# Kernel tuning notes

Hardware: AMD Instinct MI355X
Metric: run time of the kernel (lower is better)

## Reference

```python
import jax, jax.numpy as jnp
import numpy as np


def _extract_patches(img, p, s):
    # img: [B,H,W,C] -> [B,PY,PX,p,p,C]
    B, H, W, C = img.shape
    PY = (H - p) // s + 1
    PX = (W - p) // s + 1
    ar = jnp.arange(p)
    rows = jnp.arange(PY) * s
    cols = jnp.arange(PX) * s
    a = img[:, rows[:, None] + ar]              # [B,PY,p,W,C]
    b = a[:, :, :, cols[:, None] + ar]          # [B,PY,p,PX,p,C]
    return b.transpose(0, 1, 3, 2, 4, 5)


def _extract_shifted(img, int_prior, p, s):
    # img: [B,H,W,C], int_prior: [B,PY,PX,2] (dy,dx) -> shifted patches + validity
    B, H, W, C = img.shape
    _, PY, PX, _ = int_prior.shape
    ar = jnp.arange(p)
    sy = jnp.arange(PY)[None, :, None] * s + int_prior[..., 0]   # [B,PY,PX]
    sx = jnp.arange(PX)[None, None, :] * s + int_prior[..., 1]
    valid = (sy >= 0) & (sy <= H - p) & (sx >= 0) & (sx <= W - p)
    sy = jnp.clip(sy, 0, H - p)
    sx = jnp.clip(sx, 0, W - p)
    ridx = sy[..., None] + ar                                    # [B,PY,PX,p]
    cidx = sx[..., None] + ar
    bidx = jnp.arange(B)[:, None, None, None, None]
    patches = img[bidx, ridx[..., :, None], cidx[..., None, :]]  # [B,PY,PX,p,p,C]
    return patches, valid


def _patch_flow_loss(p1, p2, flow, p):
    # bilinear-warp p2 by per-patch subpixel flow and compare to p1 -> [B,PY,PX]
    ar = jnp.arange(p, dtype=flow.dtype)
    y = ar + flow[..., 0:1]                                      # [B,PY,PX,p]
    x = ar + flow[..., 1:2]
    y0 = jnp.clip(jnp.floor(y), 0, p - 1).astype(jnp.int32)
    x0 = jnp.clip(jnp.floor(x), 0, p - 1).astype(jnp.int32)
    y1 = jnp.clip(y0 + 1, 0, p - 1)
    x1 = jnp.clip(x0 + 1, 0, p - 1)
    wy = jnp.clip(y - y0, 0.0, 1.0)[..., :, None, None]
    wx = jnp.clip(x - x0, 0.0, 1.0)[..., None, :, None]
    r0 = jnp.take_along_axis(p2, y0[..., :, None, None], axis=3)
    r1 = jnp.take_along_axis(p2, y1[..., :, None, None], axis=3)
    v00 = jnp.take_along_axis(r0, x0[..., None, :, None], axis=4)
    v01 = jnp.take_along_axis(r0, x1[..., None, :, None], axis=4)
    v10 = jnp.take_along_axis(r1, x0[..., None, :, None], axis=4)
    v11 = jnp.take_along_axis(r1, x1[..., None, :, None], axis=4)
    warped = (1 - wy) * ((1 - wx) * v00 + wx * v01) + wy * ((1 - wx) * v10 + wx * v11)
    return jnp.mean((warped - p1) ** 2, axis=(3, 4, 5))


def setup_inputs() -> dict:
    key = jax.random.key(0)
    ks = jax.random.split(key, 5)
    B, H, W, C = 16, 512, 512, 3
    p, s = 16, 8
    PY = (H - p) // s + 1
    PX = (W - p) // s + 1
    hidden = 512
    din = 2 * p * p * C + 2
    img1 = jax.random.normal(ks[0], (B, H, W, C), dtype=jnp.float32)
    img2 = jax.random.normal(ks[1], (B, H, W, C), dtype=jnp.float32)
    prior = jax.random.normal(ks[2], (B, PY, PX, 2), dtype=jnp.float32) * 2.0
    w1 = jax.random.normal(ks[3], (din, hidden), dtype=jnp.float32) / np.sqrt(din)
    b1 = jnp.zeros((hidden,), jnp.float32)
    w2 = jax.random.normal(ks[4], (hidden, 2), dtype=jnp.float32) / np.sqrt(hidden)
    b2 = jnp.zeros((2,), jnp.float32)
    return {"img1": img1, "img2": img2, "prior": prior, "w1": w1, "b1": b1,
            "w2": w2, "b2": b2, "patch_size": p, "stride": s}


def reference(img1, img2, prior, w1, b1, w2, b2, patch_size, stride):
    p, s = patch_size, stride
    B, PY, PX, _ = prior.shape
    patches1 = _extract_patches(img1, p, s)                       # [B,PY,PX,p,p,C]
    int_priors = jnp.round(jax.lax.stop_gradient(prior)).astype(jnp.int32)
    remainder = prior - int_priors
    patches2, _valid = _extract_shifted(img2, int_priors, p, s)   # validity unused downstream
    N = B * PY * PX
    feat = jnp.concatenate([patches1.reshape(N, -1),
                            patches2.reshape(N, -1),
                            remainder.reshape(N, 2)], axis=-1)
    h = jax.nn.relu(feat @ w1 + b1)
    residual = (h @ w2 + b2).reshape(B, PY, PX, 2)
    remainder_flow = remainder + residual
    flow = int_priors + remainder_flow
    loss = _patch_flow_loss(patches1, patches2, remainder_flow, p)[..., None]
    return jnp.concatenate([flow, loss], axis=-1)                 # [B,PY,PX,3]
```

## Files before the change

kernel.cpp:

```cpp
#include <hip/hip_runtime.h>

#define BQ   16
#define HH   512
#define WW   512
#define CC   3
#define PSZ  16
#define STR  8
#define PYN  63
#define PXN  63
#define NPATCH (BQ * PYN * PXN)
#define HID  512
#define MT   48
#define NTH  1024
#define KSTEPS 48

typedef __attribute__((ext_vector_type(8))) short  short8;
typedef __attribute__((ext_vector_type(4))) float  f32x4;

__device__ __forceinline__ ushort f2bf(float f) {
    unsigned u = __float_as_uint(f);
    u = (u + 0x7fffu + ((u >> 16) & 1u)) >> 16;
    return (ushort)u;
}
__device__ __forceinline__ float bf2f(ushort h) {
    return __uint_as_float(((unsigned)h) << 16);
}
__device__ __forceinline__ unsigned pk2(float a, float b) {
    return (unsigned)f2bf(a) | ((unsigned)f2bf(b) << 16);
}

__global__ void pack_w1_kernel(const float* __restrict__ w1, ushort* __restrict__ w1p) {
    int e = blockIdx.x * 256 + threadIdx.x;
    int k = e >> 9;
    int n = e & 511;
    int idx = ((k >> 5) << 14) + ((n >> 4) << 9) + (((k >> 3) & 3) << 7) + ((n & 15) << 3) + (k & 7);
    w1p[idx] = f2bf(w1[e]);
}

__global__ __launch_bounds__(NTH)
void lfe_mfma_kernel(const float* __restrict__ img1,
                     const float* __restrict__ img2,
                     const float* __restrict__ prior,
                     const float* __restrict__ w1,
                     const float* __restrict__ b1,
                     const float* __restrict__ w2,
                     const float* __restrict__ b2,
                     const ushort* __restrict__ w1p,
                     float* __restrict__ out)
{
    __shared__ ushort feat[3 * KSTEPS * 512];
    __shared__ float  red[16][MT][2];
    __shared__ float  srem[MT][2];
    __shared__ float  sflow[MT][2];
    __shared__ int    sip[MT][2];
    __shared__ int    sbase1[MT];
    __shared__ int    sbase2[MT];

    const int t    = threadIdx.x;
    const int wid  = t >> 6;
    const int lane = t & 63;
    const int n0   = blockIdx.x * MT;

    const int ntb = wid << 1;
    const ushort* bbase = w1p + ((size_t)lane << 3);
    short8 B0[2], B1[2];
    #define LOADB(B, s_) {                                            \
        const ushort* p_ = bbase + ((size_t)(((s_) << 5) + ntb) << 9);\
        B[0] = *(const short8*)(p_);                                  \
        B[1] = *(const short8*)(p_ + 512);                            \
    }
    LOADB(B0, 0);
    LOADB(B1, 1);

    if (t < MT) {
        int n = n0 + t;
        float py_ = prior[(size_t)n * 2 + 0];
        float px_ = prior[(size_t)n * 2 + 1];
        int ipy = (int)rintf(py_);
        int ipx = (int)rintf(px_);
        sip[t][0] = ipy; sip[t][1] = ipx;
        srem[t][0] = py_ - (float)ipy;
        srem[t][1] = px_ - (float)ipx;
        int b  = n / (PYN * PXN);
        int r  = n % (PYN * PXN);
        int py = r / PXN, px = r % PXN;
        int by = py * STR, bx = px * STR;
        int sy = min(max(by + ipy, 0), HH - PSZ);
        int sx = min(max(bx + ipx, 0), WW - PSZ);
        sbase1[t] = ((b * HH + by) * WW + bx) * CC;
        sbase2[t] = ((b * HH + sy) * WW + sx) * CC;
    }
    __syncthreads();

    {
        const int plo = lane >> 2;
        const int kk2 = lane & 3;
        #pragma unroll 4
        for (int i = 0; i < 36; ++i) {
            int c = (i << 4) + wid;
            int m = c / 192;
            int r = c - m * 192;
            int s = r >> 2, g = r & 3;
            int pi = (m << 4) + plo;
            int ka = (s << 5) + (g << 3) + (kk2 << 1);
            const float* src;
            int e;
            if (ka < 768) { src = img1 + sbase1[pi]; e = ka; }
            else          { src = img2 + sbase2[pi]; e = ka - 768; }
            int yi  = e / 48;
            int off = e - yi * 48;
            const float* g8 = src + yi * (WW * CC) + off;
            float va = g8[0], vb = g8[1];
            int idx = ((m * KSTEPS + s) << 9) + (g << 7) + (plo << 3) + (kk2 << 1);
            *(unsigned*)(&feat[idx]) = pk2(va, vb);
        }
    }
    __syncthreads();

    const int cn = lane & 15;
    const int g  = lane >> 4;

    f32x4 acc[3][2];
    #pragma unroll
    for (int m = 0; m < 3; ++m)
        #pragma unroll
        for (int nt = 0; nt < 2; ++nt) acc[m][nt] = f32x4{0.f, 0.f, 0.f, 0.f};

    const ushort* fb = feat + lane * 8;

    for (int s = 0; s < KSTEPS; s += 2) {
        {
            short8 A0 = *(const short8*)(fb + ((0 * KSTEPS + s) << 9));
            short8 A1 = *(const short8*)(fb + ((1 * KSTEPS + s) << 9));
            short8 A2 = *(const short8*)(fb + ((2 * KSTEPS + s) << 9));
            #pragma unroll
            for (int nt = 0; nt < 2; ++nt) {
                acc[0][nt] = __builtin_amdgcn_mfma_f32_16x16x32_bf16(A0, B0[nt], acc[0][nt], 0, 0, 0);
                acc[1][nt] = __builtin_amdgcn_mfma_f32_16x16x32_bf16(A1, B0[nt], acc[1][nt], 0, 0, 0);
                acc[2][nt] = __builtin_amdgcn_mfma_f32_16x16x32_bf16(A2, B0[nt], acc[2][nt], 0, 0, 0);
            }
        }
        int sa = (s + 2 < KSTEPS) ? s + 2 : KSTEPS - 1;
        LOADB(B0, sa);
        {
            short8 A0 = *(const short8*)(fb + ((0 * KSTEPS + s + 1) << 9));
            short8 A1 = *(const short8*)(fb + ((1 * KSTEPS + s + 1) << 9));
            short8 A2 = *(const short8*)(fb + ((2 * KSTEPS + s + 1) << 9));
            #pragma unroll
            for (int nt = 0; nt < 2; ++nt) {
                acc[0][nt] = __builtin_amdgcn_mfma_f32_16x16x32_bf16(A0, B1[nt], acc[0][nt], 0, 0, 0);
                acc[1][nt] = __builtin_amdgcn_mfma_f32_16x16x32_bf16(A1, B1[nt], acc[1][nt], 0, 0, 0);
                acc[2][nt] = __builtin_amdgcn_mfma_f32_16x16x32_bf16(A2, B1[nt], acc[2][nt], 0, 0, 0);
            }
        }
        int sb = (s + 3 < KSTEPS) ? s + 3 : KSTEPS - 1;
        LOADB(B1, sb);
    }
    #undef LOADB

    float ps[3][4][2];
    #pragma unroll
    for (int m = 0; m < 3; ++m)
        #pragma unroll
        for (int r = 0; r < 4; ++r) { ps[m][r][0] = 0.f; ps[m][r][1] = 0.f; }

    #pragma unroll
    for (int nt = 0; nt < 2; ++nt) {
        int j = (wid << 5) + (nt << 4) + cn;
        float w1a = w1[(size_t)1536 * HID + j];
        float w1b = w1[(size_t)1537 * HID + j];
        float bb  = b1[j];
        float w20 = w2[(size_t)j * 2 + 0];
        float w21 = w2[(size_t)j * 2 + 1];
        #pragma unroll
        for (int m = 0; m < 3; ++m) {
            #pragma unroll
            for (int r = 0; r < 4; ++r) {
                int pr = (m << 4) + (g << 2) + r;
                float h = acc[m][nt][r] + bb + srem[pr][0] * w1a + srem[pr][1] * w1b;
                h = fmaxf(h, 0.f);
                ps[m][r][0] = fmaf(h, w20, ps[m][r][0]);
                ps[m][r][1] = fmaf(h, w21, ps[m][r][1]);
            }
        }
    }
    #pragma unroll
    for (int m = 0; m < 3; ++m)
        #pragma unroll
        for (int r = 0; r < 4; ++r)
            #pragma unroll
            for (int cc = 0; cc < 2; ++cc)
                #pragma unroll
                for (int off = 1; off < 16; off <<= 1)
                    ps[m][r][cc] += __shfl_xor(ps[m][r][cc], off, 64);
    if (cn == 0) {
        #pragma unroll
        for (int m = 0; m < 3; ++m)
            #pragma unroll
            for (int r = 0; r < 4; ++r) {
                int pr = (m << 4) + (g << 2) + r;
                red[wid][pr][0] = ps[m][r][0];
                red[wid][pr][1] = ps[m][r][1];
            }
    }
    __syncthreads();
    if (t < MT * 2) {
        int pr = t >> 1, c = t & 1;
        float v = b2[c];
        #pragma unroll
        for (int w = 0; w < 16; ++w) v += red[w][pr][c];
        sflow[pr][c] = srem[pr][c] + v;
    }
    __syncthreads();

    {
        const int gi = t >> 4, lt = t & 15;
        if (gi < MT) {
            const int pi = gi;
            const float rfy = sflow[pi][0], rfx = sflow[pi][1];
            const int pbase = (pi >> 4) * 24576 + ((pi & 15) << 3);
            float lsum = 0.f;

            const int xj = lt;
            float x  = (float)xj + rfx;
            int   x0 = min(max((int)floorf(x), 0), PSZ - 1);
            int   x1 = min(x0 + 1, PSZ - 1);
            float wx = fminf(fmaxf(x - (float)x0, 0.f), 1.f);
            int   c0 = x0 * 3, c1 = x1 * 3;
            #pragma unroll 4
            for (int yi = 0; yi < PSZ; ++yi) {
                float y  = (float)yi + rfy;
                int   y0 = min(max((int)floorf(y), 0), PSZ - 1);
                int   y1 = min(y0 + 1, PSZ - 1);
                float wy = fminf(fmaxf(y - (float)y0, 0.f), 1.f);
                int r0 = 768 + y0 * 48, r1 = 768 + y1 * 48;
                int ep = yi * 48 + xj * 3;
                #pragma unroll
                for (int cc = 0; cc < 3; ++cc) {
                    int k00 = r0 + c0 + cc, k01 = r0 + c1 + cc;
                    int k10 = r1 + c0 + cc, k11 = r1 + c1 + cc;
                    float v00 = bf2f(feat[pbase + ((k00 >> 3) << 7) + (k00 & 7)]);
                    float v01 = bf2f(feat[pbase + ((k01 >> 3) << 7) + (k01 & 7)]);
                    float v10 = bf2f(feat[pbase + ((k10 >> 3) << 7) + (k10 & 7)]);
                    float v11 = bf2f(feat[pbase + ((k11 >> 3) << 7) + (k11 & 7)]);
                    float a = v00 + wx * (v01 - v00);
                    float b = v10 + wx * (v11 - v10);
                    float warped = a + wy * (b - a);
                    int kp = ep + cc;
                    float d = warped - bf2f(feat[pbase + ((kp >> 3) << 7) + (kp & 7)]);
                    lsum = fmaf(d, d, lsum);
                }
            }
            #pragma unroll
            for (int off = 1; off < 16; off <<= 1)
                lsum += __shfl_xor(lsum, off, 64);

            if (lt == 0) {
                int n = n0 + pi;
                out[(size_t)n * 3 + 0] = (float)sip[pi][0] + rfy;
                out[(size_t)n * 3 + 1] = (float)sip[pi][1] + rfx;
                out[(size_t)n * 3 + 2] = lsum * (1.f / 768.f);
            }
        }
    }
}

extern "C" void kernel_launch(void* const* d_in, const int* in_sizes, int n_in,
                              void* d_out, int out_size, void* d_ws, size_t ws_size,
                              hipStream_t stream) {
    const float* img1  = (const float*)d_in[0];
    const float* img2  = (const float*)d_in[1];
    const float* prior = (const float*)d_in[2];
    const float* w1    = (const float*)d_in[3];
    const float* b1    = (const float*)d_in[4];
    const float* w2    = (const float*)d_in[5];
    const float* b2    = (const float*)d_in[6];
    float* out = (float*)d_out;
    ushort* w1p = (ushort*)d_ws;

    pack_w1_kernel<<<dim3((1536 * HID) / 256), dim3(256), 0, stream>>>(w1, w1p);

    dim3 grid(NPATCH / MT);
    dim3 block(NTH);
    lfe_mfma_kernel<<<grid, block, 0, stream>>>(img1, img2, prior, w1, b1, w2, b2, w1p, out);
}
```

Before: 403.5 us.

## Halve patches per block with XOR-swizzled LDS layout and split loss rows

The patch tile per block drops from 48 to 24. The LDS feature buffer shrinks and is laid out as one 16-row tile plus a half-height 8-row tile, so fewer MFMA and A-loads run per k-step and more blocks can fit per CU. An XOR swizzle is added to the LDS feature indices to cut bank conflicts on A-fragment reads and on the warp-loss gathers. The loss stage now spreads each patch over 32 threads, splitting the rows in halves. In exchange, each w1 B fragment is reused across fewer patches, so global/L2 traffic for weights doubles per patch, and the second MFMA tile wastes half its rows.

```diff
diff --git a/kernel.cpp b/kernel.cpp
--- a/kernel.cpp
+++ b/kernel.cpp
@@ -10,9 +10,10 @@
 #define PXN  63
 #define NPATCH (BQ * PYN * PXN)
 #define HID  512
-#define MT   48
+#define MT   24
 #define NTH  1024
 #define KSTEPS 48
+#define M1BASE 24576
 
 typedef __attribute__((ext_vector_type(8))) short  short8;
 typedef __attribute__((ext_vector_type(4))) float  f32x4;
@@ -27,6 +28,12 @@
 }
 __device__ __forceinline__ unsigned pk2(float a, float b) {
     return (unsigned)f2bf(a) | ((unsigned)f2bf(b) << 16);
+}
+
+__device__ __forceinline__ int fidx(int pi, int k) {
+    int B = k >> 3, kk = k & 7;
+    if (pi < 16) return (B << 7) + ((pi ^ (B & 15)) << 3) + kk;
+    return M1BASE + (B << 6) + (((pi - 16) ^ (B & 7)) << 3) + kk;
 }
 
 __global__ void pack_w1_kernel(const float* __restrict__ w1, ushort* __restrict__ w1p) {
@@ -37,7 +44,7 @@
     w1p[idx] = f2bf(w1[e]);
 }
 
-__global__ __launch_bounds__(NTH)
+__global__ __launch_bounds__(NTH, 8)
 void lfe_mfma_kernel(const float* __restrict__ img1,
                      const float* __restrict__ img2,
                      const float* __restrict__ prior,
@@ -48,7 +55,7 @@
                      const ushort* __restrict__ w1p,
                      float* __restrict__ out)
 {
-    __shared__ ushort feat[3 * KSTEPS * 512];
+    __shared__ ushort feat[36864];
     __shared__ float  red[16][MT][2];
     __shared__ float  srem[MT][2];
     __shared__ float  sflow[MT][2];
@@ -64,10 +71,10 @@
     const int ntb = wid << 1;
     const ushort* bbase = w1p + ((size_t)lane << 3);
     short8 B0[2], B1[2];
-    #define LOADB(B, s_) {                                            \
+    #define LOADB(Bv, s_) {                                           \
         const ushort* p_ = bbase + ((size_t)(((s_) << 5) + ntb) << 9);\
-        B[0] = *(const short8*)(p_);                                  \
-        B[1] = *(const short8*)(p_ + 512);                            \
+        Bv[0] = *(const short8*)(p_);                                 \
+        Bv[1] = *(const short8*)(p_ + 512);                           \
     }
     LOADB(B0, 0);
     LOADB(B1, 1);
@@ -96,23 +103,33 @@
         const int plo = lane >> 2;
         const int kk2 = lane & 3;
         #pragma unroll 4
-        for (int i = 0; i < 36; ++i) {
-            int c = (i << 4) + wid;
-            int m = c / 192;
-            int r = c - m * 192;
-            int s = r >> 2, g = r & 3;
-            int pi = (m << 4) + plo;
-            int ka = (s << 5) + (g << 3) + (kk2 << 1);
-            const float* src;
-            int e;
-            if (ka < 768) { src = img1 + sbase1[pi]; e = ka; }
-            else          { src = img2 + sbase2[pi]; e = ka - 768; }
-            int yi  = e / 48;
-            int off = e - yi * 48;
-            const float* g8 = src + yi * (WW * CC) + off;
-            float va = g8[0], vb = g8[1];
-            int idx = ((m * KSTEPS + s) << 9) + (g << 7) + (plo << 3) + (kk2 << 1);
-            *(unsigned*)(&feat[idx]) = pk2(va, vb);
+        for (int i = 0; i < 24; ++i) {
+            int c  = (i << 4) + wid;
+            int m1 = (c >= 192);
+            int r  = c - (m1 ? 192 : 0);
+            int s  = r >> 2, g = r & 3;
+            int Bb = (s << 2) + g;
+            bool active = true;
+            int pi, idx;
+            if (!m1) {
+                pi  = plo;
+                idx = (s << 9) + (g << 7) + (((plo) ^ (Bb & 15)) << 3) + (kk2 << 1);
+            } else {
+                active = (plo < 8);
+                pi  = 16 + (plo & 7);
+                idx = M1BASE + (s << 8) + (g << 6) + ((((plo) & 7) ^ (Bb & 7)) << 3) + (kk2 << 1);
+            }
+            if (active) {
+                int ka = (s << 5) + (g << 3) + (kk2 << 1);
+                const float* src;
+                int e;
+                if (ka < 768) { src = img1 + sbase1[pi]; e = ka; }
+                else          { src = img2 + sbase2[pi]; e = ka - 768; }
+                int yi  = e / 48;
+                int off = e - yi * 48;
+                const float* g8 = src + yi * (WW * CC) + off;
+                *(unsigned*)(&feat[idx]) = pk2(g8[0], g8[1]);
+            }
         }
     }
     __syncthreads();
@@ -120,37 +137,34 @@
     const int cn = lane & 15;
     const int g  = lane >> 4;
 
-    f32x4 acc[3][2];
+    f32x4 acc[2][2];
     #pragma unroll
-    for (int m = 0; m < 3; ++m)
+    for (int m = 0; m < 2; ++m)
         #pragma unroll
         for (int nt = 0; nt < 2; ++nt) acc[m][nt] = f32x4{0.f, 0.f, 0.f, 0.f};
-
-    const ushort* fb = feat + lane * 8;
 
     for (int s = 0; s < KSTEPS; s += 2) {
         {
-            short8 A0 = *(const short8*)(fb + ((0 * KSTEPS + s) << 9));
-            short8 A1 = *(const short8*)(fb + ((1 * KSTEPS + s) << 9));
-            short8 A2 = *(const short8*)(fb + ((2 * KSTEPS + s) << 9));
+            int Bb = (s << 2) + g;
+            short8 A0 = *(const short8*)(feat + (s << 9) + (g << 7) + ((cn ^ (Bb & 15)) << 3));
+            short8 A1 = *(const short8*)(feat + M1BASE + (s << 8) + (g << 6) + (((lane & 7) ^ (Bb & 7)) << 3));
             #pragma unroll
             for (int nt = 0; nt < 2; ++nt) {
                 acc[0][nt] = __builtin_amdgcn_mfma_f32_16x16x32_bf16(A0, B0[nt], acc[0][nt], 0, 0, 0);
                 acc[1][nt] = __builtin_amdgcn_mfma_f32_16x16x32_bf16(A1, B0[nt], acc[1][nt], 0, 0, 0);
-                acc[2][nt] = __builtin_amdgcn_mfma_f32_16x16x32_bf16(A2, B0[nt], acc[2][nt], 0, 0, 0);
             }
         }
         int sa = (s + 2 < KSTEPS) ? s + 2 : KSTEPS - 1;
         LOADB(B0, sa);
         {
-            short8 A0 = *(const short8*)(fb + ((0 * KSTEPS + s + 1) << 9));
-            short8 A1 = *(const short8*)(fb + ((1 * KSTEPS + s + 1) << 9));
-            short8 A2 = *(const short8*)(fb + ((2 * KSTEPS + s + 1) << 9));
+            int s1 = s + 1;
+            int Bb = (s1 << 2) + g;
+            short8 A0 = *(const short8*)(feat + (s1 << 9) + (g << 7) + ((cn ^ (Bb & 15)) << 3));
+            short8 A1 = *(const short8*)(feat + M1BASE + (s1 << 8) + (g << 6) + (((lane & 7) ^ (Bb & 7)) << 3));
             #pragma unroll
             for (int nt = 0; nt < 2; ++nt) {
                 acc[0][nt] = __builtin_amdgcn_mfma_f32_16x16x32_bf16(A0, B1[nt], acc[0][nt], 0, 0, 0);
                 acc[1][nt] = __builtin_amdgcn_mfma_f32_16x16x32_bf16(A1, B1[nt], acc[1][nt], 0, 0, 0);
-                acc[2][nt] = __builtin_amdgcn_mfma_f32_16x16x32_bf16(A2, B1[nt], acc[2][nt], 0, 0, 0);
             }
         }
         int sb = (s + 3 < KSTEPS) ? s + 3 : KSTEPS - 1;
@@ -158,9 +172,9 @@
     }
     #undef LOADB
 
-    float ps[3][4][2];
+    float ps[2][4][2];
     #pragma unroll
-    for (int m = 0; m < 3; ++m)
+    for (int m = 0; m < 2; ++m)
         #pragma unroll
         for (int r = 0; r < 4; ++r) { ps[m][r][0] = 0.f; ps[m][r][1] = 0.f; }
 
@@ -173,19 +187,21 @@
         float w20 = w2[(size_t)j * 2 + 0];
         float w21 = w2[(size_t)j * 2 + 1];
         #pragma unroll
-        for (int m = 0; m < 3; ++m) {
+        for (int m = 0; m < 2; ++m) {
             #pragma unroll
             for (int r = 0; r < 4; ++r) {
                 int pr = (m << 4) + (g << 2) + r;
-                float h = acc[m][nt][r] + bb + srem[pr][0] * w1a + srem[pr][1] * w1b;
-                h = fmaxf(h, 0.f);
-                ps[m][r][0] = fmaf(h, w20, ps[m][r][0]);
-                ps[m][r][1] = fmaf(h, w21, ps[m][r][1]);
+                if (pr < MT) {
+                    float h = acc[m][nt][r] + bb + srem[pr][0] * w1a + srem[pr][1] * w1b;
+                    h = fmaxf(h, 0.f);
+                    ps[m][r][0] = fmaf(h, w20, ps[m][r][0]);
+                    ps[m][r][1] = fmaf(h, w21, ps[m][r][1]);
+                }
             }
         }
     }
     #pragma unroll
-    for (int m = 0; m < 3; ++m)
+    for (int m = 0; m < 2; ++m)
         #pragma unroll
         for (int r = 0; r < 4; ++r)
             #pragma unroll
@@ -195,12 +211,14 @@
                     ps[m][r][cc] += __shfl_xor(ps[m][r][cc], off, 64);
     if (cn == 0) {
         #pragma unroll
-        for (int m = 0; m < 3; ++m)
+        for (int m = 0; m < 2; ++m)
             #pragma unroll
             for (int r = 0; r < 4; ++r) {
                 int pr = (m << 4) + (g << 2) + r;
-                red[wid][pr][0] = ps[m][r][0];
-                red[wid][pr][1] = ps[m][r][1];
+                if (pr < MT) {
+                    red[wid][pr][0] = ps[m][r][0];
+                    red[wid][pr][1] = ps[m][r][1];
+                }
             }
     }
     __syncthreads();
@@ -214,21 +232,24 @@
     __syncthreads();
 
     {
-        const int gi = t >> 4, lt = t & 15;
+        const int gi = t >> 5;
+        const int lt = t & 31;
         if (gi < MT) {
             const int pi = gi;
             const float rfy = sflow[pi][0], rfx = sflow[pi][1];
-            const int pbase = (pi >> 4) * 24576 + ((pi & 15) << 3);
-            float lsum = 0.f;
-
-            const int xj = lt;
+            const int xj = lt & 15;
+            const int yh = lt >> 4;
+
             float x  = (float)xj + rfx;
             int   x0 = min(max((int)floorf(x), 0), PSZ - 1);
             int   x1 = min(x0 + 1, PSZ - 1);
             float wx = fminf(fmaxf(x - (float)x0, 0.f), 1.f);
             int   c0 = x0 * 3, c1 = x1 * 3;
-            #pragma unroll 4
-            for (int yi = 0; yi < PSZ; ++yi) {
+
+            float lsum = 0.f;
+            #pragma unroll
+            for (int yy = 0; yy < 8; ++yy) {
+                int yi = (yh << 3) + yy;
                 float y  = (float)yi + rfy;
                 int   y0 = min(max((int)floorf(y), 0), PSZ - 1);
                 int   y1 = min(y0 + 1, PSZ - 1);
@@ -237,22 +258,19 @@
                 int ep = yi * 48 + xj * 3;
                 #pragma unroll
                 for (int cc = 0; cc < 3; ++cc) {
-                    int k00 = r0 + c0 + cc, k01 = r0 + c1 + cc;
-                    int k10 = r1 + c0 + cc, k11 = r1 + c1 + cc;
-                    float v00 = bf2f(feat[pbase + ((k00 >> 3) << 7) + (k00 & 7)]);
-                    float v01 = bf2f(feat[pbase + ((k01 >> 3) << 7) + (k01 & 7)]);
-                    float v10 = bf2f(feat[pbase + ((k10 >> 3) << 7) + (k10 & 7)]);
-                    float v11 = bf2f(feat[pbase + ((k11 >> 3) << 7) + (k11 & 7)]);
+                    float v00 = bf2f(feat[fidx(pi, r0 + c0 + cc)]);
+                    float v01 = bf2f(feat[fidx(pi, r0 + c1 + cc)]);
+                    float v10 = bf2f(feat[fidx(pi, r1 + c0 + cc)]);
+                    float v11 = bf2f(feat[fidx(pi, r1 + c1 + cc)]);
                     float a = v00 + wx * (v01 - v00);
                     float b = v10 + wx * (v11 - v10);
                     float warped = a + wy * (b - a);
-                    int kp = ep + cc;
-                    float d = warped - bf2f(feat[pbase + ((kp >> 3) << 7) + (kp & 7)]);
+                    float d = warped - bf2f(feat[fidx(pi, ep + cc)]);
                     lsum = fmaf(d, d, lsum);
                 }
             }
             #pragma unroll
-            for (int off = 1; off < 16; off <<= 1)
+            for (int off = 1; off < 32; off <<= 1)
                 lsum += __shfl_xor(lsum, off, 64);
 
             if (lt == 0) {
```

Result: slower. 587.0 us (+45.5%).
